# Performance work log

Measured on AMD Instinct MI355X. Metric: run time of the kernel, lower is better.

The kernel has to match this reference:

```python
import jax, jax.numpy as jnp
import numpy as np

N, E, H, MID = 4096, 384, 6, 96  # n_refs, embed_dim, num_heads, mlp mid dim (max(E//4,32))
DH = E // H  # head dim = 64


def setup_inputs() -> dict:
    key = jax.random.key(0)
    ks = jax.random.split(key, 12)
    def w(k, shape, fan_in):
        return jax.random.normal(k, shape, jnp.float32) / np.float32(np.sqrt(fan_in))
    return {
        "low": jax.random.normal(ks[0], (N, E), jnp.float32),
        "high": jax.random.normal(ks[1], (N, E), jnp.float32),
        "ref_w": jax.random.uniform(ks[2], (N,), jnp.float32) + 0.1,
        "low_w1": w(ks[3], (E, MID), E), "low_b1": jnp.zeros((MID,), jnp.float32),
        "low_w2": w(ks[4], (MID, E), MID), "low_b2": jnp.zeros((E,), jnp.float32),
        "high_w1": w(ks[5], (E, MID), E), "high_b1": jnp.zeros((MID,), jnp.float32),
        "high_w2": w(ks[6], (MID, E), MID), "high_b2": jnp.zeros((E,), jnp.float32),
        "layer_fuse": jnp.array([0.4, 0.6], jnp.float32),
        "wqkv": w(ks[7], (E, 3 * E), E), "bqkv": jnp.zeros((3 * E,), jnp.float32),
        "wo": w(ks[8], (E, E), E), "bo": jnp.zeros((E,), jnp.float32),
        "ln_g": jnp.ones((E,), jnp.float32), "ln_b": jnp.zeros((E,), jnp.float32),
    }


def _channel_mlp(x, w1, b1, w2, b2):
    h = jax.nn.gelu(x @ w1 + b1, approximate=False)  # [N, MID]
    return x * jax.nn.sigmoid(h @ w2 + b2)           # [N, E]


def _forward(low, high, ref_w, low_w1, low_b1, low_w2, low_b2,
             high_w1, high_b1, high_w2, high_b2, layer_fuse,
             wqkv, bqkv, wo, bo, ln_g, ln_b):
    lw = jax.nn.softmax(layer_fuse)
    fused = lw[0] * _channel_mlp(low, low_w1, low_b1, low_w2, low_b2) \
          + lw[1] * _channel_mlp(high, high_w1, high_b1, high_w2, high_b2)  # [N, E]
    # single-layer MHA over the n-reference sequence (batch of 1, batch_first)
    qkv = fused @ wqkv + bqkv                      # [N, 3E]
    q, k, v = jnp.split(qkv, 3, axis=-1)
    q = q.reshape(N, H, DH).transpose(1, 0, 2)     # [H, N, DH]
    k = k.reshape(N, H, DH).transpose(1, 0, 2)
    v = v.reshape(N, H, DH).transpose(1, 0, 2)
    scores = jnp.einsum("hnd,hmd->hnm", q, k) / np.float32(np.sqrt(DH))
    attn = jax.nn.softmax(scores, axis=-1)         # [H, N, N]
    ctx = jnp.einsum("hnm,hmd->hnd", attn, v)      # [H, N, DH]
    attn_out = ctx.transpose(1, 0, 2).reshape(N, E) @ wo + bo
    x = attn_out + fused                           # residual
    mu = jnp.mean(x, axis=-1, keepdims=True)
    var = jnp.mean(jnp.square(x - mu), axis=-1, keepdims=True)
    x = (x - mu) / jnp.sqrt(var + 1e-5) * ln_g + ln_b
    w = ref_w / jnp.sum(ref_w)
    res = jnp.sum(x * w[:, None], axis=0)          # weighted mean over refs -> [E]
    return res / (jnp.linalg.norm(res) + 1e-8)


def reference(low, high, ref_w, low_w1, low_b1, low_w2, low_b2,
              high_w1, high_b1, high_w2, high_b2, layer_fuse,
              wqkv, bqkv, wo, bo, ln_g, ln_b):
    return _forward(low, high, ref_w, low_w1, low_b1, low_w2, low_b2,
                    high_w1, high_b1, high_w2, high_b2, layer_fuse,
                    wqkv, bqkv, wo, bo, ln_g, ln_b)
```

## Files before the change

### kernel.cpp

```cpp
#include <hip/hip_runtime.h>
#include <math.h>

#define Nn 4096
#define Ee 384
#define Hh 6
#define DHh 64
#define MIDm 96
#define TEe 1152
#define SPLIT 8

typedef short s16x8 __attribute__((ext_vector_type(8)));
typedef float f32x4 __attribute__((ext_vector_type(4)));
typedef float f32x16 __attribute__((ext_vector_type(16)));
typedef unsigned short ushort_t;
typedef unsigned short ushort4_t __attribute__((ext_vector_type(4)));

#define CROW(r, hf) ((((r) & 3)) + 8 * ((r) >> 2) + 4 * (hf))

__device__ __forceinline__ float gelu_exact(float x) {
    return 0.5f * x * (1.0f + erff(x * 0.70710678118654752f));
}
__device__ __forceinline__ float sigmoidf_(float x) {
    return 1.0f / (1.0f + __expf(-x));
}
__device__ __forceinline__ ushort_t f2bf(float x) {
    unsigned int u = __float_as_uint(x);
    u = (u + 0x7FFFu + ((u >> 16) & 1u)) >> 16;
    return (ushort_t)u;
}
__device__ __forceinline__ float bf2f(ushort_t u) {
    return __uint_as_float(((unsigned int)u) << 16);
}
__device__ __forceinline__ unsigned int cvtpk(float a, float b) {
    unsigned int r;
    asm("v_cvt_pk_bf16_f32 %0, %1, %2" : "=v"(r) : "v"(a), "v"(b));
    return r;
}

#define W1L_OFF 0
#define W1H_OFF 36864
#define W2L_OFF 73728
#define W2H_OFF 110592
#define WQKV_OFF 147456
#define WO_OFF 589824

__global__ __launch_bounds__(256) void k_cvt(
    const float* __restrict__ lw1, const float* __restrict__ hw1,
    const float* __restrict__ lw2, const float* __restrict__ hw2,
    const float* __restrict__ wqkv, const float* __restrict__ wo,
    ushort_t* __restrict__ wT) {
    __shared__ float tl[32][33];
    const int b = blockIdx.x;
    const float* src;
    int R, C, doff, ti;
    if (b < 36)       { src = lw1;  R = 384; C = 96;   doff = W1L_OFF;  ti = b; }
    else if (b < 72)  { src = hw1;  R = 384; C = 96;   doff = W1H_OFF;  ti = b - 36; }
    else if (b < 108) { src = lw2;  R = 96;  C = 384;  doff = W2L_OFF;  ti = b - 72; }
    else if (b < 144) { src = hw2;  R = 96;  C = 384;  doff = W2H_OFF;  ti = b - 108; }
    else if (b < 576) { src = wqkv; R = 384; C = 1152; doff = WQKV_OFF; ti = b - 144; }
    else              { src = wo;   R = 384; C = 384;  doff = WO_OFF;   ti = b - 576; }
    const int tcn = C >> 5;
    const int tr = ti / tcn, tc = ti % tcn;
    const int col = threadIdx.x & 31, r8 = threadIdx.x >> 5;
#pragma unroll
    for (int i = 0; i < 4; i++) {
        const int row = r8 + 8 * i;
        tl[row][col] = src[(size_t)(tr * 32 + row) * C + tc * 32 + col];
    }
    __syncthreads();
#pragma unroll
    for (int i = 0; i < 4; i++) {
        const int rowp = r8 + 8 * i;
        wT[doff + (size_t)(tc * 32 + rowp) * R + tr * 32 + col] = f2bf(tl[col][rowp]);
    }
}

__global__ __launch_bounds__(256) void k_mlp(
    const float* __restrict__ low, const float* __restrict__ high,
    const float* __restrict__ lf, const ushort_t* __restrict__ wT,
    const float* __restrict__ lb1, const float* __restrict__ lb2,
    const float* __restrict__ hb1, const float* __restrict__ hb2,
    ushort_t* __restrict__ fusedb) {
    __shared__ float redsg[6144];
    __shared__ ushort_t Hs[2][16][104];
    float* red = redsg;
    ushort_t* Sg = (ushort_t*)redsg;
    const int t = threadIdx.x;
    const int w = t >> 6, l = t & 63, l15 = l & 15, g4 = l >> 4;
    const int st = w >> 1, kh = w & 1;
    const int rb = blockIdx.x * 16;
    const float* Xf = st ? high : low;
    const ushort_t* w1T = wT + (st ? W1H_OFF : W1L_OFF);
    const ushort_t* w2T = wT + (st ? W2H_OFF : W2L_OFF);
    {
        f32x4 hA[6];
#pragma unroll
        for (int nt = 0; nt < 6; nt++) hA[nt] = (f32x4){0.f, 0.f, 0.f, 0.f};
        for (int ks = 0; ks < 6; ks++) {
            const float* ap = &Xf[(size_t)(rb + l15) * 384 + kh * 192 + ks * 32 + g4 * 8];
            f32x4 a0 = *(const f32x4*)ap;
            f32x4 a1 = *(const f32x4*)(ap + 4);
            union { unsigned int uw[4]; s16x8 v; } ua;
            ua.uw[0] = cvtpk(a0[0], a0[1]);
            ua.uw[1] = cvtpk(a0[2], a0[3]);
            ua.uw[2] = cvtpk(a1[0], a1[1]);
            ua.uw[3] = cvtpk(a1[2], a1[3]);
#pragma unroll
            for (int nt = 0; nt < 6; nt++) {
                s16x8 bf = *(const s16x8*)&w1T[(nt * 16 + l15) * 384 + kh * 192 + ks * 32 + g4 * 8];
                hA[nt] = __builtin_amdgcn_mfma_f32_16x16x32_bf16(ua.v, bf, hA[nt], 0, 0, 0);
            }
        }
#pragma unroll
        for (int nt = 0; nt < 6; nt++)
#pragma unroll
            for (int r = 0; r < 4; r++)
                red[((st * 2 + kh) * 16 + g4 * 4 + r) * 96 + nt * 16 + l15] = hA[nt][r];
    }
    __syncthreads();
    for (int idx = t; idx < 2 * 16 * 96; idx += 256) {
        const int st2 = idx / 1536, rem = idx % 1536;
        const int rowm = rem / 96, mc = rem % 96;
        const float v = red[((st2 * 2) * 16 + rowm) * 96 + mc] +
                        red[((st2 * 2 + 1) * 16 + rowm) * 96 + mc] +
                        (st2 ? hb1[mc] : lb1[mc]);
        Hs[st2][rowm][mc] = f2bf(gelu_exact(v));
    }
    __syncthreads();
    {
        const float* b2p = st ? hb2 : lb2;
        f32x4 sA[12];
#pragma unroll
        for (int nt = 0; nt < 12; nt++) sA[nt] = (f32x4){0.f, 0.f, 0.f, 0.f};
#pragma unroll
        for (int ks = 0; ks < 3; ks++) {
            s16x8 af = *(const s16x8*)&Hs[st][l15][ks * 32 + g4 * 8];
#pragma unroll
            for (int nt = 0; nt < 12; nt++) {
                s16x8 bf = *(const s16x8*)&w2T[(kh * 192 + nt * 16 + l15) * 96 + ks * 32 + g4 * 8];
                sA[nt] = __builtin_amdgcn_mfma_f32_16x16x32_bf16(af, bf, sA[nt], 0, 0, 0);
            }
        }
#pragma unroll
        for (int nt = 0; nt < 12; nt++) {
            const float bb = b2p[kh * 192 + nt * 16 + l15];
#pragma unroll
            for (int r = 0; r < 4; r++)
                Sg[(st * 16 + g4 * 4 + r) * 384 + kh * 192 + nt * 16 + l15] =
                    f2bf(sigmoidf_(sA[nt][r] + bb));
        }
    }
    __syncthreads();
    {
        const float a0 = lf[0], a1 = lf[1];
        const float mx = fmaxf(a0, a1);
        const float e0 = __expf(a0 - mx), e1 = __expf(a1 - mx);
        const float inv = 1.0f / (e0 + e1);
        const float w0 = e0 * inv, w1v = e1 * inv;
        for (int base = t * 4; base < 16 * 384; base += 256 * 4) {
            const int row = base / 384, e0i = base % 384;
            const int gr = rb + row;
            f32x4 lo4 = *(const f32x4*)&low[(size_t)gr * 384 + e0i];
            f32x4 hi4 = *(const f32x4*)&high[(size_t)gr * 384 + e0i];
            ushort4_t s0 = *(const ushort4_t*)&Sg[row * 384 + e0i];
            ushort4_t s1 = *(const ushort4_t*)&Sg[(16 + row) * 384 + e0i];
            ushort4_t fb;
#pragma unroll
            for (int i = 0; i < 4; i++)
                fb[i] = f2bf(w0 * lo4[i] * bf2f(s0[i]) + w1v * hi4[i] * bf2f(s1[i]));
            *(ushort4_t*)&fusedb[(size_t)gr * 384 + e0i] = fb;
        }
    }
}

__global__ __launch_bounds__(256) void k_qkv(
    const ushort_t* __restrict__ fusedb, const ushort_t* __restrict__ wT,
    const float* __restrict__ bqkv,
    ushort_t* __restrict__ qb, ushort_t* __restrict__ kb, ushort_t* __restrict__ vtb) {
    __shared__ float tls[4][32][40];
    const int t = threadIdx.x;
    const int w = t >> 6, l = t & 63, ll = l & 31, hf = l >> 5;
    const int mh = w >> 1, nh = w & 1;
    const int rb = blockIdx.x * 64 + mh * 32;
    const int cb = blockIdx.y * 192 + nh * 96;
    const ushort_t* wq = wT + WQKV_OFF;
    f32x16 acc[3];
#pragma unroll
    for (int nt = 0; nt < 3; nt++)
#pragma unroll
        for (int r = 0; r < 16; r++) acc[nt][r] = 0.0f;
    for (int ks = 0; ks < 24; ks++) {
        s16x8 af = *(const s16x8*)&fusedb[(size_t)(rb + ll) * 384 + ks * 16 + hf * 8];
#pragma unroll
        for (int nt = 0; nt < 3; nt++) {
            s16x8 bf = *(const s16x8*)&wq[(size_t)(cb + nt * 32 + ll) * 384 + ks * 16 + hf * 8];
            acc[nt] = __builtin_amdgcn_mfma_f32_32x32x16_bf16(af, bf, acc[nt], 0, 0, 0);
        }
    }
#pragma unroll
    for (int nt = 0; nt < 3; nt++) {
        const int nb = cb + nt * 32;
        const int which = nb / 384, wn = nb % 384;
        const int hb = wn >> 6, d0 = wn & 63;
        const float bias = bqkv[nb + ll];
        if (which == 2) {
            const int d = d0 + ll;
#pragma unroll
            for (int g2 = 0; g2 < 4; g2++) {
                ushort4_t u4;
#pragma unroll
                for (int i2 = 0; i2 < 4; i2++) u4[i2] = f2bf(acc[nt][g2 * 4 + i2] + bias);
                *(ushort4_t*)&vtb[((size_t)(hb * 64 + d)) * Nn + rb + 8 * g2 + 4 * hf] = u4;
            }
        } else {
            const float sc = (which == 0) ? 0.18033688f : 1.0f;
#pragma unroll
            for (int r = 0; r < 16; r++) tls[w][CROW(r, hf)][ll] = (acc[nt][r] + bias) * sc;
            ushort_t* dst = which ? kb : qb;
            const int row2 = l >> 1, sg = l & 1;
            union { ushort_t us[16]; s16x8 v[2]; } u;
#pragma unroll
            for (int j = 0; j < 16; j++) u.us[j] = f2bf(tls[w][row2][sg * 16 + j]);
            size_t base = ((size_t)hb * Nn + rb + row2) * 64 + d0 + sg * 16;
            *(s16x8*)&dst[base] = u.v[0];
            *(s16x8*)&dst[base + 8] = u.v[1];
        }
    }
}

__global__ __launch_bounds__(256) void k_attn(
    const ushort_t* __restrict__ qb, const ushort_t* __restrict__ kb,
    const ushort_t* __restrict__ vtb, ushort_t* __restrict__ pof,
    float* __restrict__ pml) {
    __shared__ ushort_t Kt[2][4096];
    __shared__ ushort_t Vt[2][4096];
    const int t = threadIdx.x;
    const int wid = t >> 6, l = t & 63, ll = l & 31, hf = l >> 5;
    const int lid = blockIdx.x;
    const int xcd = lid & 7, gi = lid >> 3;
    const int pair = xcd * 6 + (gi >> 5);
    const int qt = gi & 31;
    const int h = pair % Hh, sp = pair / Hh;
    const int qrow0 = qt * 128 + wid * 32;
    const int srow = t >> 3, scol = (t & 7) * 8;
    const int soff0 = srow * 64 + (scol ^ ((srow & 7) << 3));
    const int srow1 = srow + 32;
    const int soff1 = srow1 * 64 + (scol ^ ((srow1 & 7) << 3));
    const ushort_t* kbase = kb + (size_t)h * Nn * DHh;
    const ushort_t* vbase = vtb + (size_t)h * DHh * Nn;
    const int kst0 = sp * (Nn / SPLIT);
#define NT (Nn / (64 * SPLIT))
    s16x8 kr0, kr1, vr0, vr1;
#define AISSUE(TI) { const int ktb = kst0 + (TI) * 64;                                  \
        kr0 = *(const s16x8*)&kbase[(size_t)(ktb + srow) * DHh + scol];                  \
        kr1 = *(const s16x8*)&kbase[(size_t)(ktb + srow1) * DHh + scol];                 \
        vr0 = *(const s16x8*)&vbase[(size_t)srow * Nn + ktb + scol];                     \
        vr1 = *(const s16x8*)&vbase[(size_t)srow1 * Nn + ktb + scol]; }
#define AWRITE(B) {                                                                      \
        *(s16x8*)&Kt[B][soff0] = kr0; *(s16x8*)&Kt[B][soff1] = kr1;                      \
        *(s16x8*)&Vt[B][soff0] = vr0; *(s16x8*)&Vt[B][soff1] = vr1; }

    s16x8 qf[4];
#pragma unroll
    for (int dc = 0; dc < 4; dc++)
        qf[dc] = *(const s16x8*)&qb[((size_t)h * Nn + qrow0 + ll) * DHh + dc * 16 + hf * 8];
    f32x16 o0, o1;
#pragma unroll
    for (int r = 0; r < 16; r++) { o0[r] = 0.0f; o1[r] = 0.0f; }
    float lsum = 0.0f;
    const int xorl = (ll & 7) << 3;

    AISSUE(0);
    AWRITE(0);
    __syncthreads();
    for (int kt = 0; kt < NT; kt++) {
        const int cur = kt & 1;
        if (kt < NT - 1) AISSUE(kt + 1);
        const ushort_t* KtC = Kt[cur];
        const ushort_t* VtC = Vt[cur];
        f32x16 s0, s1;
#pragma unroll
        for (int r = 0; r < 16; r++) { s0[r] = 0.0f; s1[r] = 0.0f; }
        __builtin_amdgcn_s_setprio(1);
#pragma unroll
        for (int dc = 0; dc < 4; dc++) {
            const int colE = dc * 16 + hf * 8;
            s16x8 kf0 = *(const s16x8*)&KtC[ll * 64 + (colE ^ xorl)];
            s16x8 kf1 = *(const s16x8*)&KtC[(32 + ll) * 64 + (colE ^ xorl)];
            s0 = __builtin_amdgcn_mfma_f32_32x32x16_bf16(kf0, qf[dc], s0, 0, 0, 0);
            s1 = __builtin_amdgcn_mfma_f32_32x32x16_bf16(kf1, qf[dc], s1, 0, 0, 0);
        }
        __builtin_amdgcn_s_setprio(0);
#pragma unroll
        for (int r = 0; r < 16; r++) { s0[r] = exp2f(s0[r]); lsum += s0[r]; }
#pragma unroll
        for (int r = 0; r < 16; r++) { s1[r] = exp2f(s1[r]); lsum += s1[r]; }
#pragma unroll
        for (int ks = 0; ks < 4; ks++) {
            const f32x16 S = (ks < 2) ? s0 : s1;
            const int b = (ks & 1) * 8;
            unsigned int t1 = cvtpk(S[b + 0], S[b + 1]);
            unsigned int t3 = cvtpk(S[b + 2], S[b + 3]);
            unsigned int t2 = cvtpk(S[b + 4], S[b + 5]);
            unsigned int t4 = cvtpk(S[b + 6], S[b + 7]);
            asm("v_permlane32_swap_b32 %0, %1" : "+v"(t1), "+v"(t2));
            asm("v_permlane32_swap_b32 %0, %1" : "+v"(t3), "+v"(t4));
            union { unsigned int uw[4]; s16x8 v; } u;
            u.uw[0] = t1;
            u.uw[1] = t3;
            u.uw[2] = t2;
            u.uw[3] = t4;
            const int colE = ks * 16 + hf * 8;
            s16x8 vf0 = *(const s16x8*)&VtC[ll * 64 + (colE ^ xorl)];
            s16x8 vf1 = *(const s16x8*)&VtC[(32 + ll) * 64 + (colE ^ xorl)];
            o0 = __builtin_amdgcn_mfma_f32_32x32x16_bf16(vf0, u.v, o0, 0, 0, 0);
            o1 = __builtin_amdgcn_mfma_f32_32x32x16_bf16(vf1, u.v, o1, 0, 0, 0);
        }
        __syncthreads();
        if (kt < NT - 1) {
            AWRITE(cur ^ 1);
            __syncthreads();
        }
    }
    lsum += __shfl_xor(lsum, 32, 64);
#pragma unroll
    for (int r = 0; r < 16; r++) {
        const int d_a = CROW(r, hf), d_b = 32 + CROW(r, hf);
        pof[((size_t)(sp * Ee + h * 64 + d_a)) * Nn + qrow0 + ll] = f2bf(o0[r]);
        pof[((size_t)(sp * Ee + h * 64 + d_b)) * Nn + qrow0 + ll] = f2bf(o1[r]);
    }
    if (hf == 0)
        pml[((size_t)sp * Hh + h) * Nn + qrow0 + ll] = lsum;
#undef AISSUE
#undef AWRITE
#undef NT
}

__global__ __launch_bounds__(256) void k_merge(
    const ushort_t* __restrict__ pof, const float* __restrict__ pml,
    ushort_t* __restrict__ ctxb) {
    __shared__ float lsums[SPLIT][Hh][64];
    __shared__ float dinv[Hh][64];
    __shared__ ushort_t tile[64][96];
    const int t = threadIdx.x;
    const int qb0 = blockIdx.x * 64;
    const int eq = blockIdx.y;
    for (int i = t; i < SPLIT * Hh * 64; i += 256) {
        const int s = i / (Hh * 64), r2 = i % (Hh * 64);
        const int hh = r2 / 64, qq = r2 % 64;
        lsums[s][hh][qq] = pml[((size_t)s * Hh + hh) * Nn + qb0 + qq];
    }
    __syncthreads();
    for (int i = t; i < Hh * 64; i += 256) {
        const int hh = i / 64, qq = i % 64;
        float den = 0.0f;
#pragma unroll
        for (int s = 0; s < SPLIT; s++) den += lsums[s][hh][qq];
        dinv[hh][qq] = 1.0f / den;
    }
    __syncthreads();
    const int qq = t & 63, e0 = t >> 6;
    for (int i = 0; i < 24; i++) {
        const int el = e0 + 4 * i;
        const int e = eq * 96 + el;
        const int hh = e >> 6;
        float acc = 0.0f;
#pragma unroll
        for (int s = 0; s < SPLIT; s++)
            acc += bf2f(pof[((size_t)(s * Ee + e)) * Nn + qb0 + qq]);
        tile[qq][el] = f2bf(acc * dinv[hh][qq]);
    }
    __syncthreads();
    for (int i = t; i < 64 * 12; i += 256) {
        const int q2 = i / 12, sg = i % 12;
        *(s16x8*)&ctxb[((size_t)(qb0 + q2)) * 384 + eq * 96 + sg * 8] =
            *(const s16x8*)&tile[q2][sg * 8];
    }
}

__global__ __launch_bounds__(256) void k_oln(
    const ushort_t* __restrict__ ctxb, const ushort_t* __restrict__ wT,
    const float* __restrict__ bo, const ushort_t* __restrict__ fusedb,
    const float* __restrict__ lng, const float* __restrict__ lnb,
    const float* __restrict__ rw, float* __restrict__ part) {
    __shared__ float xs[16][388];
    __shared__ float stats[16][2];
    const int t = threadIdx.x;
    const int w = t >> 6, l = t & 63, l15 = l & 15, g4 = l >> 4;
    const int rb = blockIdx.x * 16;
    const ushort_t* woT = wT + WO_OFF;
    f32x4 oA[6];
#pragma unroll
    for (int nt = 0; nt < 6; nt++) oA[nt] = (f32x4){0.f, 0.f, 0.f, 0.f};
    for (int ks = 0; ks < 12; ks++) {
        s16x8 af = *(const s16x8*)&ctxb[(size_t)(rb + l15) * 384 + ks * 32 + g4 * 8];
#pragma unroll
        for (int nt = 0; nt < 6; nt++) {
            s16x8 bf = *(const s16x8*)&woT[(size_t)(w * 96 + nt * 16 + l15) * 384 + ks * 32 + g4 * 8];
            oA[nt] = __builtin_amdgcn_mfma_f32_16x16x32_bf16(af, bf, oA[nt], 0, 0, 0);
        }
    }
#pragma unroll
    for (int nt = 0; nt < 6; nt++) {
        const int col = w * 96 + nt * 16 + l15;
        const float bias = bo[col];
#pragma unroll
        for (int r = 0; r < 4; r++) {
            const int row = g4 * 4 + r;
            xs[row][col] = oA[nt][r] + bias + bf2f(fusedb[(size_t)(rb + row) * 384 + col]);
        }
    }
    __syncthreads();
    {
        const int row = t >> 4, j = t & 15;
        float s1 = 0.0f, s2 = 0.0f;
        for (int i = 0; i < 24; i++) {
            const float x = xs[row][j + 16 * i];
            s1 += x;
            s2 += x * x;
        }
#pragma unroll
        for (int off = 1; off < 16; off <<= 1) {
            s1 += __shfl_xor(s1, off, 64);
            s2 += __shfl_xor(s2, off, 64);
        }
        if (j == 0) {
            const float mu = s1 * (1.0f / Ee);
            const float var = s2 * (1.0f / Ee) - mu * mu;
            stats[row][0] = mu;
            stats[row][1] = rsqrtf(var + 1e-5f);
        }
    }
    __syncthreads();
    for (int c = t; c < 384; c += 256) {
        const float gt = lng[c], bb = lnb[c];
        float acc = 0.0f;
        for (int r = 0; r < 16; r++) {
            const float xn = (xs[r][c] - stats[r][0]) * stats[r][1] * gt + bb;
            acc += xn * rw[rb + r];
        }
        part[(size_t)blockIdx.x * Ee + c] = acc;
    }
}

__global__ __launch_bounds__(384) void k_final(const float* __restrict__ part,
                                               const float* __restrict__ rw,
                                               float* __restrict__ outp) {
    __shared__ float red[6], redw[6];
    const int t = threadIdx.x;
    float s = 0.0f;
    for (int b = 0; b < 256; b++) s += part[(size_t)b * Ee + t];
    float wsp = 0.0f;
    for (int i = t; i < Nn; i += 384) wsp += rw[i];
    float q2 = s * s;
#pragma unroll
    for (int off = 32; off > 0; off >>= 1) {
        q2 += __shfl_down(q2, off, 64);
        wsp += __shfl_down(wsp, off, 64);
    }
    const int wid = t >> 6, lane = t & 63;
    if (lane == 0) { red[wid] = q2; redw[wid] = wsp; }
    __syncthreads();
    float tot = 0.0f, wtot = 0.0f;
#pragma unroll
    for (int w = 0; w < 6; w++) { tot += red[w]; wtot += redw[w]; }
    outp[t] = s / (sqrtf(tot) + 1e-8f * wtot);
}

extern "C" void kernel_launch(void* const* d_in, const int* in_sizes, int n_in,
                              void* d_out, int out_size, void* d_ws, size_t ws_size,
                              hipStream_t stream) {
    const float* low  = (const float*)d_in[0];
    const float* high = (const float*)d_in[1];
    const float* rw   = (const float*)d_in[2];
    const float* lw1  = (const float*)d_in[3];
    const float* lb1  = (const float*)d_in[4];
    const float* lw2  = (const float*)d_in[5];
    const float* lb2  = (const float*)d_in[6];
    const float* hw1  = (const float*)d_in[7];
    const float* hb1  = (const float*)d_in[8];
    const float* hw2  = (const float*)d_in[9];
    const float* hb2  = (const float*)d_in[10];
    const float* lf   = (const float*)d_in[11];
    const float* wqkv = (const float*)d_in[12];
    const float* bqkv = (const float*)d_in[13];
    const float* wo   = (const float*)d_in[14];
    const float* bo   = (const float*)d_in[15];
    const float* lng  = (const float*)d_in[16];
    const float* lnb  = (const float*)d_in[17];

    float* ws = (float*)d_ws;
    const size_t NE = (size_t)Nn * Ee;
    float* pml  = ws;
    float* part = ws + 196608;
    ushort_t* u16base = (ushort_t*)(ws + 294912);
    ushort_t* fusedb = u16base;
    ushort_t* vtb    = u16base + NE;
    ushort_t* qb     = u16base + 2 * NE;
    ushort_t* kb     = u16base + 3 * NE;
    ushort_t* ctxb   = u16base + 4 * NE;
    ushort_t* wT     = u16base + 5 * NE;
    ushort_t* pof    = wT + 737280;

    hipLaunchKernelGGL(k_cvt, dim3(720), dim3(256), 0, stream,
                       lw1, hw1, lw2, hw2, wqkv, wo, wT);
    hipLaunchKernelGGL(k_mlp, dim3(256), dim3(256), 0, stream,
                       low, high, lf, wT, lb1, lb2, hb1, hb2, fusedb);
    hipLaunchKernelGGL(k_qkv, dim3(64, 6), dim3(256), 0, stream,
                       fusedb, wT, bqkv, qb, kb, vtb);
    hipLaunchKernelGGL(k_attn, dim3(Hh * SPLIT * 32), dim3(256), 0, stream,
                       qb, kb, vtb, pof, pml);
    hipLaunchKernelGGL(k_merge, dim3(64, 4), dim3(256), 0, stream, pof, pml, ctxb);
    hipLaunchKernelGGL(k_oln, dim3(256), dim3(256), 0, stream,
                       ctxb, wT, bo, fusedb, lng, lnb, rw, part);
    hipLaunchKernelGGL(k_final, dim3(1), dim3(384), 0, stream, part, rw, (float*)d_out);
}
```

Before: 149.4 us.

## Fuse split-K merge into output-projection kernel and widen attention blocks to 512 threads

The separate k_merge kernel is removed. Each k_oln block now reduces the split partial attention outputs and denominators for its 16 rows directly into a swizzled LDS tile, which is then fed to the Wo MFMA. This drops one kernel launch and the write and re-read of the ctx buffer. Separately, k_attn now uses 512-thread blocks covering 256 query rows, so each K/V tile loaded into LDS is shared by twice as many waves and each thread loads half as much. The cost is fewer attention blocks and more per-block LDS pressure, and k_oln does more work before it can start its MFMA.

```diff
diff --git a/kernel.cpp b/kernel.cpp
--- a/kernel.cpp
+++ b/kernel.cpp
@@ -228,37 +228,31 @@
     }
 }
 
-__global__ __launch_bounds__(256) void k_attn(
+__global__ __launch_bounds__(512) void k_attn(
     const ushort_t* __restrict__ qb, const ushort_t* __restrict__ kb,
     const ushort_t* __restrict__ vtb, ushort_t* __restrict__ pof,
     float* __restrict__ pml) {
     __shared__ ushort_t Kt[2][4096];
     __shared__ ushort_t Vt[2][4096];
     const int t = threadIdx.x;
-    const int wid = t >> 6, l = t & 63, ll = l & 31, hf = l >> 5;
+    const int wid8 = t >> 6, l = t & 63, ll = l & 31, hf = l >> 5;
     const int lid = blockIdx.x;
     const int xcd = lid & 7, gi = lid >> 3;
-    const int pair = xcd * 6 + (gi >> 5);
-    const int qt = gi & 31;
+    const int pair = xcd * 6 + (gi >> 4);
+    const int qt = gi & 15;
     const int h = pair % Hh, sp = pair / Hh;
-    const int qrow0 = qt * 128 + wid * 32;
+    const int qrow0 = qt * 256 + wid8 * 32;
     const int srow = t >> 3, scol = (t & 7) * 8;
-    const int soff0 = srow * 64 + (scol ^ ((srow & 7) << 3));
-    const int srow1 = srow + 32;
-    const int soff1 = srow1 * 64 + (scol ^ ((srow1 & 7) << 3));
+    const int soff = srow * 64 + (scol ^ ((srow & 7) << 3));
     const ushort_t* kbase = kb + (size_t)h * Nn * DHh;
     const ushort_t* vbase = vtb + (size_t)h * DHh * Nn;
     const int kst0 = sp * (Nn / SPLIT);
 #define NT (Nn / (64 * SPLIT))
-    s16x8 kr0, kr1, vr0, vr1;
-#define AISSUE(TI) { const int ktb = kst0 + (TI) * 64;                                  \
+    s16x8 kr0, vr0;
+#define AISSUE(TI) { const int ktb = kst0 + (TI) * 64;                                   \
         kr0 = *(const s16x8*)&kbase[(size_t)(ktb + srow) * DHh + scol];                  \
-        kr1 = *(const s16x8*)&kbase[(size_t)(ktb + srow1) * DHh + scol];                 \
-        vr0 = *(const s16x8*)&vbase[(size_t)srow * Nn + ktb + scol];                     \
-        vr1 = *(const s16x8*)&vbase[(size_t)srow1 * Nn + ktb + scol]; }
-#define AWRITE(B) {                                                                      \
-        *(s16x8*)&Kt[B][soff0] = kr0; *(s16x8*)&Kt[B][soff1] = kr1;                      \
-        *(s16x8*)&Vt[B][soff0] = vr0; *(s16x8*)&Vt[B][soff1] = vr1; }
+        vr0 = *(const s16x8*)&vbase[(size_t)srow * Nn + ktb + scol]; }
+#define AWRITE(B) { *(s16x8*)&Kt[B][soff] = kr0; *(s16x8*)&Vt[B][soff] = vr0; }
 
     s16x8 qf[4];
 #pragma unroll
@@ -336,64 +330,54 @@
 #undef NT
 }
 
-__global__ __launch_bounds__(256) void k_merge(
+__global__ __launch_bounds__(256) void k_oln(
     const ushort_t* __restrict__ pof, const float* __restrict__ pml,
-    ushort_t* __restrict__ ctxb) {
-    __shared__ float lsums[SPLIT][Hh][64];
-    __shared__ float dinv[Hh][64];
-    __shared__ ushort_t tile[64][96];
-    const int t = threadIdx.x;
-    const int qb0 = blockIdx.x * 64;
-    const int eq = blockIdx.y;
-    for (int i = t; i < SPLIT * Hh * 64; i += 256) {
-        const int s = i / (Hh * 64), r2 = i % (Hh * 64);
-        const int hh = r2 / 64, qq = r2 % 64;
-        lsums[s][hh][qq] = pml[((size_t)s * Hh + hh) * Nn + qb0 + qq];
-    }
-    __syncthreads();
-    for (int i = t; i < Hh * 64; i += 256) {
-        const int hh = i / 64, qq = i % 64;
-        float den = 0.0f;
-#pragma unroll
-        for (int s = 0; s < SPLIT; s++) den += lsums[s][hh][qq];
-        dinv[hh][qq] = 1.0f / den;
-    }
-    __syncthreads();
-    const int qq = t & 63, e0 = t >> 6;
-    for (int i = 0; i < 24; i++) {
-        const int el = e0 + 4 * i;
-        const int e = eq * 96 + el;
-        const int hh = e >> 6;
-        float acc = 0.0f;
-#pragma unroll
-        for (int s = 0; s < SPLIT; s++)
-            acc += bf2f(pof[((size_t)(s * Ee + e)) * Nn + qb0 + qq]);
-        tile[qq][el] = f2bf(acc * dinv[hh][qq]);
-    }
-    __syncthreads();
-    for (int i = t; i < 64 * 12; i += 256) {
-        const int q2 = i / 12, sg = i % 12;
-        *(s16x8*)&ctxb[((size_t)(qb0 + q2)) * 384 + eq * 96 + sg * 8] =
-            *(const s16x8*)&tile[q2][sg * 8];
-    }
-}
-
-__global__ __launch_bounds__(256) void k_oln(
-    const ushort_t* __restrict__ ctxb, const ushort_t* __restrict__ wT,
-    const float* __restrict__ bo, const ushort_t* __restrict__ fusedb,
+    const ushort_t* __restrict__ wT, const float* __restrict__ bo,
+    const ushort_t* __restrict__ fusedb,
     const float* __restrict__ lng, const float* __restrict__ lnb,
     const float* __restrict__ rw, float* __restrict__ part) {
+    __shared__ ushort_t cx[16][384];
     __shared__ float xs[16][388];
     __shared__ float stats[16][2];
+    __shared__ float dinvs[Hh][16];
     const int t = threadIdx.x;
     const int w = t >> 6, l = t & 63, l15 = l & 15, g4 = l >> 4;
     const int rb = blockIdx.x * 16;
+    if (t < Hh * 16) {
+        const int hh = t >> 4, qq = t & 15;
+        float den = 0.0f;
+#pragma unroll
+        for (int s = 0; s < SPLIT; s++)
+            den += pml[((size_t)s * Hh + hh) * Nn + rb + qq];
+        dinvs[hh][qq] = 1.0f / den;
+    }
+    __syncthreads();
+    for (int task = t; task < 768; task += 256) {
+        const int e = task >> 1, half = task & 1;
+        const int hh = e >> 6;
+        float a8[8];
+#pragma unroll
+        for (int j = 0; j < 8; j++) a8[j] = 0.0f;
+#pragma unroll
+        for (int s = 0; s < SPLIT; s++) {
+            s16x8 v = *(const s16x8*)&pof[((size_t)(s * Ee + e)) * Nn + rb + half * 8];
+#pragma unroll
+            for (int j = 0; j < 8; j++) a8[j] += bf2f((ushort_t)v[j]);
+        }
+#pragma unroll
+        for (int j = 0; j < 8; j++) {
+            const int q = half * 8 + j;
+            cx[q][e ^ ((q & 7) << 3)] = f2bf(a8[j] * dinvs[hh][q]);
+        }
+    }
+    __syncthreads();
     const ushort_t* woT = wT + WO_OFF;
     f32x4 oA[6];
 #pragma unroll
     for (int nt = 0; nt < 6; nt++) oA[nt] = (f32x4){0.f, 0.f, 0.f, 0.f};
+    const int xo = (l15 & 7) << 3;
     for (int ks = 0; ks < 12; ks++) {
-        s16x8 af = *(const s16x8*)&ctxb[(size_t)(rb + l15) * 384 + ks * 32 + g4 * 8];
+        s16x8 af = *(const s16x8*)&cx[l15][(ks * 32 + g4 * 8) ^ xo];
 #pragma unroll
         for (int nt = 0; nt < 6; nt++) {
             s16x8 bf = *(const s16x8*)&woT[(size_t)(w * 96 + nt * 16 + l15) * 384 + ks * 32 + g4 * 8];
@@ -498,8 +482,7 @@
     ushort_t* vtb    = u16base + NE;
     ushort_t* qb     = u16base + 2 * NE;
     ushort_t* kb     = u16base + 3 * NE;
-    ushort_t* ctxb   = u16base + 4 * NE;
-    ushort_t* wT     = u16base + 5 * NE;
+    ushort_t* wT     = u16base + 4 * NE;
     ushort_t* pof    = wT + 737280;
 
     hipLaunchKernelGGL(k_cvt, dim3(720), dim3(256), 0, stream,
@@ -508,10 +491,9 @@
                        low, high, lf, wT, lb1, lb2, hb1, hb2, fusedb);
     hipLaunchKernelGGL(k_qkv, dim3(64, 6), dim3(256), 0, stream,
                        fusedb, wT, bqkv, qb, kb, vtb);
-    hipLaunchKernelGGL(k_attn, dim3(Hh * SPLIT * 32), dim3(256), 0, stream,
+    hipLaunchKernelGGL(k_attn, dim3(Hh * SPLIT * 16), dim3(512), 0, stream,
                        qb, kb, vtb, pof, pml);
-    hipLaunchKernelGGL(k_merge, dim3(64, 4), dim3(256), 0, stream, pof, pml, ctxb);
     hipLaunchKernelGGL(k_oln, dim3(256), dim3(256), 0, stream,
-                       ctxb, wT, bo, fusedb, lng, lnb, rw, part);
+                       pof, pml, wT, bo, fusedb, lng, lnb, rw, part);
     hipLaunchKernelGGL(k_final, dim3(1), dim3(384), 0, stream, part, rw, (float*)d_out);
 }
```

Measured after the change: 139.6 us. 1.07x faster.
